# Optimization experiments

Hardware: AMD Instinct MI355X
Metric: run time of the kernel (lower is better)

## Reference

```python
import jax, jax.numpy as jnp
import numpy as np

B, NELEC, D, NION = 2048, 32, 128, 8
NSPIN = 2
NS = NELEC // NSPIN  # electrons (= orbitals) per spin


def setup_inputs() -> dict:
    key = jax.random.key(0)
    ks = jax.random.split(key, 6)
    eq_inputs = jax.random.normal(ks[0], (B, NELEC, D), dtype=jnp.float32)
    r_ei = jax.random.normal(ks[1], (B, NELEC, NION, 3), dtype=jnp.float32)
    W = jax.random.normal(ks[2], (NSPIN, D, NS), dtype=jnp.float32) / np.sqrt(D).astype(np.float32)
    b = jax.random.normal(ks[3], (NSPIN, NS), dtype=jnp.float32) * 0.1
    env_a = jax.random.normal(ks[4], (NSPIN, NION, NS), dtype=jnp.float32) * 0.5 + 1.0
    env_ion = jax.random.normal(ks[5], (NSPIN, NION, NS), dtype=jnp.float32) / np.sqrt(NION).astype(np.float32)
    return {"eq_inputs": eq_inputs, "r_ei": r_ei, "W": W, "b": b,
            "env_a": env_a, "env_ion": env_ion}


def _submatrix_row_indices(n):
    # idx[i, j] = row index kept at slot j after deleting row i
    j = np.arange(n - 1)
    idx = j[None, :] + (j[None, :] >= np.arange(n)[:, None])
    return jnp.asarray(idx)  # (n, n-1) int32


def reference(eq_inputs, r_ei, W, b, env_a, env_ion):
    # split into spins (equal split -> stack for vectorization)
    eq_s = jnp.stack(jnp.split(eq_inputs, NSPIN, axis=-2))   # (s,B,ns,d)
    rei_s = jnp.stack(jnp.split(r_ei, NSPIN, axis=-3))       # (s,B,ns,nion,3)

    # FermiNet orbital layer: linear part * isotropic exponential envelope
    linear = jnp.einsum("sbnd,sdo->sbno", eq_s, W) + b[:, None, None, :]
    dist = jnp.linalg.norm(rei_s, axis=-1)                   # (s,B,ns,nion)
    # exp(-||a (r - R)||) = exp(-|a| * ||r - R||) for isotropic scalar decay a
    exp_part = jnp.exp(-dist[..., None] * jnp.abs(env_a)[:, None, None, :, :])
    env = jnp.einsum("sbnio,sio->sbno", exp_part, env_ion)
    M = linear * env                                         # (s,B,ns,ns) square orbital matrices

    # slog cofactor antiequivariance along first column
    first = M[..., 0]                                        # (s,B,ns)
    osign = jnp.sign(first)
    olog = jnp.log(jnp.abs(first))
    y = M[..., 1:]                                           # delete column 0
    idx = _submatrix_row_indices(NS)
    sub = jnp.take(y, idx, axis=-2)                          # (s,B,ns,ns-1,ns-1): row i deleted
    csign, clog = jnp.linalg.slogdet(sub)                    # (s,B,ns)
    alt = jnp.asarray((-1.0) ** np.arange(NS), dtype=M.dtype)  # alternating signs (-1)^i
    a_sign = osign * csign * alt
    a_log = olog + clog

    # multiply equivariant inputs (slog form) by the per-particle antisymmetry
    out_sign = jnp.sign(eq_s) * a_sign[..., None]            # (s,B,ns,d)
    out_log = jnp.log(jnp.abs(eq_s)) + a_log[..., None]
    # stacked representation of the per-spin SLArrayList: (spin, {sign,log}, B, ns, d)
    return jnp.stack([out_sign, out_log], axis=1)
```

## Files before the change

### kernel.cpp

```cpp
#include <hip/hip_runtime.h>
#include <math.h>

#define NB 2048

__device__ __forceinline__ float signf_(float x) {
    return (x > 0.0f) ? 1.0f : ((x < 0.0f) ? -1.0f : 0.0f);
}

__global__ __launch_bounds__(256, 3)
void slogcof_kernel(const float* __restrict__ eq,
                    const float* __restrict__ rei,
                    const float* __restrict__ Wm,
                    const float* __restrict__ bias,
                    const float* __restrict__ env_a,
                    const float* __restrict__ env_ion,
                    float* __restrict__ out)
{
    __shared__ float  sEq[4][16][132];
    __shared__ double sM[4][16][18];
    __shared__ double sDist[4][16][8];
    __shared__ float  sA[4][2][16];

    const int tid = threadIdx.x;
    const int w   = tid >> 6;
    const int l   = tid & 63;
    const int P   = blockIdx.x * 4 + w;
    const int s   = P >> 11;
    const int bb  = P & (NB - 1);

    const int o16 = l & 15;
    const int q4  = l >> 4;

    const float* eqp = eq + (size_t)bb * 4096 + s * 2048;
    #pragma unroll
    for (int it = 0; it < 8; ++it) {
        const int idx = it * 256 + l * 4;
        const float4 v = *reinterpret_cast<const float4*>(eqp + idx);
        *reinterpret_cast<float4*>(&sEq[w][idx >> 7][idx & 127]) = v;
    }

    #pragma unroll
    for (int rep = 0; rep < 2; ++rep) {
        const int n = (l >> 3) + rep * 8;
        const int i = l & 7;
        const float* rp = rei + (size_t)bb * 768 + s * 384 + n * 24 + i * 3;
        const double x = (double)rp[0], y = (double)rp[1], z = (double)rp[2];
        sDist[w][n][i] = sqrt(x * x + y * y + z * z);
    }

    __syncthreads();

    double accv[4] = {0.0, 0.0, 0.0, 0.0};
    {
        const float* Wp = Wm + s * 2048;
        #pragma unroll 4
        for (int d0 = 0; d0 < 128; d0 += 4) {
            const float4 a0 = *reinterpret_cast<const float4*>(&sEq[w][4 * q4 + 0][d0]);
            const float4 a1 = *reinterpret_cast<const float4*>(&sEq[w][4 * q4 + 1][d0]);
            const float4 a2 = *reinterpret_cast<const float4*>(&sEq[w][4 * q4 + 2][d0]);
            const float4 a3 = *reinterpret_cast<const float4*>(&sEq[w][4 * q4 + 3][d0]);
            const double w0 = (double)Wp[(d0 + 0) * 16 + o16];
            const double w1 = (double)Wp[(d0 + 1) * 16 + o16];
            const double w2 = (double)Wp[(d0 + 2) * 16 + o16];
            const double w3 = (double)Wp[(d0 + 3) * 16 + o16];
            accv[0] += (double)a0.x * w0 + (double)a0.y * w1 + (double)a0.z * w2 + (double)a0.w * w3;
            accv[1] += (double)a1.x * w0 + (double)a1.y * w1 + (double)a1.z * w2 + (double)a1.w * w3;
            accv[2] += (double)a2.x * w0 + (double)a2.y * w1 + (double)a2.z * w2 + (double)a2.w * w3;
            accv[3] += (double)a3.x * w0 + (double)a3.y * w1 + (double)a3.z * w2 + (double)a3.w * w3;
        }
    }

    {
        const double bd = (double)bias[s * 16 + o16];
        double ev[4] = {0.0, 0.0, 0.0, 0.0};
        #pragma unroll
        for (int i = 0; i < 8; ++i) {
            const double ea = fabs((double)env_a[s * 128 + i * 16 + o16]);
            const double ei = (double)env_ion[s * 128 + i * 16 + o16];
            #pragma unroll
            for (int j = 0; j < 4; ++j)
                ev[j] += exp(-sDist[w][4 * q4 + j][i] * ea) * ei;
        }
        #pragma unroll
        for (int j = 0; j < 4; ++j)
            sM[w][4 * q4 + j][o16] = (accv[j] + bd) * ev[j];
    }
    __syncthreads();

    if (w == 0) {
        const int g = q4;
        const int j = o16;
        double row[16];
        #pragma unroll
        for (int c = 0; c < 16; ++c) row[c] = sM[g][j][c];
        const double m0 = row[0];

        double logdet = 0.0;
        int dsign = 1;
        int used = 0;
        int mystep = -1;

        #pragma unroll
        for (int k = 0; k < 16; ++k) {
            unsigned key;
            {
                const float av = (float)fabs(row[k]);
                key = used ? (unsigned)j
                           : ((__float_as_uint(av) & 0xFFFFFFC0u) | 0x20u | (unsigned)j);
            }
            #pragma unroll
            for (int off = 8; off >= 1; off >>= 1) {
                const unsigned k2 = (unsigned)__shfl_xor((int)key, off, 16);
                if (k2 > key) key = k2;
            }
            const int p = (int)(key & 15u);
            const double pivv = __shfl(row[k], p, 16);
            logdet += (double)logf((float)fabs(pivv));
            if (pivv < 0.0) dsign = -dsign;
            else if (pivv == 0.0) dsign = 0;
            if (j == p) { used = 1; mystep = k; }
            const double minv = (pivv != 0.0) ? (1.0 / pivv) : 0.0;
            const double mul = row[k] * minv;
            const int upd = !used;
            #pragma unroll
            for (int c = k + 1; c < 16; ++c) {
                const double pv = __shfl(row[c], p, 16);
                if (upd) row[c] -= mul * pv;
            }
            if (upd) row[k] = mul;
        }

        int invc = 0;
        #pragma unroll
        for (int j2 = 0; j2 < 16; ++j2) {
            const int s2 = __shfl(mystep, j2, 16);
            if (j2 > j && mystep > s2) invc++;
        }
        #pragma unroll
        for (int off = 8; off >= 1; off >>= 1) invc += __shfl_xor(invc, off, 16);
        if (invc & 1) dsign = -dsign;

        double wv = 0.0;
        #pragma unroll
        for (int o = 0; o < 16; ++o) {
            double c0 = (mystep < o) ? (row[o] * wv) : 0.0;
            #pragma unroll
            for (int off = 8; off >= 1; off >>= 1) c0 += __shfl_xor(c0, off, 16);
            if (mystep == o) wv = (((o == 0) ? 1.0 : 0.0) - c0) / row[o];
        }
        double vv = 0.0;
        #pragma unroll
        for (int k = 15; k >= 0; --k) {
            double c0 = (mystep > k) ? (row[k] * vv) : 0.0;
            #pragma unroll
            for (int off = 8; off >= 1; off >>= 1) c0 += __shfl_xor(c0, off, 16);
            if (mystep == k) vv = wv - c0;
        }

        const double zj = vv;
        const float zs = (zj > 0.0) ? 1.0f : ((zj < 0.0) ? -1.0f : 0.0f);
        const float ms = (m0 > 0.0) ? 1.0f : ((m0 < 0.0) ? -1.0f : 0.0f);
        sA[g][0][j] = ms * (float)dsign * zs;
        sA[g][1][j] = logf((float)fabs(m0)) + (float)logdet + logf((float)fabs(zj));
    }
    __syncthreads();

    float* op0 = out + (size_t)s * 8388608 + (size_t)bb * 2048;
    float* op1 = op0 + 4194304;
    #pragma unroll
    for (int it = 0; it < 8; ++it) {
        const int n  = it * 2 + (l >> 5);
        const int d0 = (l & 31) * 4;
        const float4 x = *reinterpret_cast<const float4*>(&sEq[w][n][d0]);
        const float a_s = sA[w][0][n];
        const float a_l = sA[w][1][n];
        float4 osg, olg;
        osg.x = signf_(x.x) * a_s;  olg.x = logf(fabsf(x.x)) + a_l;
        osg.y = signf_(x.y) * a_s;  olg.y = logf(fabsf(x.y)) + a_l;
        osg.z = signf_(x.z) * a_s;  olg.z = logf(fabsf(x.z)) + a_l;
        osg.w = signf_(x.w) * a_s;  olg.w = logf(fabsf(x.w)) + a_l;
        *reinterpret_cast<float4*>(op0 + n * 128 + d0) = osg;
        *reinterpret_cast<float4*>(op1 + n * 128 + d0) = olg;
    }
}

extern "C" void kernel_launch(void* const* d_in, const int* in_sizes, int n_in,
                              void* d_out, int out_size, void* d_ws, size_t ws_size,
                              hipStream_t stream) {
    (void)in_sizes; (void)n_in; (void)out_size; (void)d_ws; (void)ws_size;
    slogcof_kernel<<<dim3(1024), dim3(256), 0, stream>>>(
        (const float*)d_in[0],
        (const float*)d_in[1],
        (const float*)d_in[2],
        (const float*)d_in[3],
        (const float*)d_in[4],
        (const float*)d_in[5],
        (float*)d_out);
}
```

Before: 143.6 us.

## Drop LDS staging of eq inputs, read from global, and spread determinant across waves

Measured after the change: 152.6 us. 6.3% more time.

```diff
diff --git a/kernel.cpp b/kernel.cpp
--- a/kernel.cpp
+++ b/kernel.cpp
@@ -7,7 +7,7 @@
     return (x > 0.0f) ? 1.0f : ((x < 0.0f) ? -1.0f : 0.0f);
 }
 
-__global__ __launch_bounds__(256, 3)
+__global__ __launch_bounds__(256, 4)
 void slogcof_kernel(const float* __restrict__ eq,
                     const float* __restrict__ rei,
                     const float* __restrict__ Wm,
@@ -16,7 +16,6 @@
                     const float* __restrict__ env_ion,
                     float* __restrict__ out)
 {
-    __shared__ float  sEq[4][16][132];
     __shared__ double sM[4][16][18];
     __shared__ double sDist[4][16][8];
     __shared__ float  sA[4][2][16];
@@ -32,12 +31,6 @@
     const int q4  = l >> 4;
 
     const float* eqp = eq + (size_t)bb * 4096 + s * 2048;
-    #pragma unroll
-    for (int it = 0; it < 8; ++it) {
-        const int idx = it * 256 + l * 4;
-        const float4 v = *reinterpret_cast<const float4*>(eqp + idx);
-        *reinterpret_cast<float4*>(&sEq[w][idx >> 7][idx & 127]) = v;
-    }
 
     #pragma unroll
     for (int rep = 0; rep < 2; ++rep) {
@@ -47,18 +40,21 @@
         const double x = (double)rp[0], y = (double)rp[1], z = (double)rp[2];
         sDist[w][n][i] = sqrt(x * x + y * y + z * z);
     }
-
     __syncthreads();
 
     double accv[4] = {0.0, 0.0, 0.0, 0.0};
     {
         const float* Wp = Wm + s * 2048;
+        const float* r0 = eqp + (4 * q4 + 0) * 128;
+        const float* r1 = eqp + (4 * q4 + 1) * 128;
+        const float* r2 = eqp + (4 * q4 + 2) * 128;
+        const float* r3 = eqp + (4 * q4 + 3) * 128;
         #pragma unroll 4
         for (int d0 = 0; d0 < 128; d0 += 4) {
-            const float4 a0 = *reinterpret_cast<const float4*>(&sEq[w][4 * q4 + 0][d0]);
-            const float4 a1 = *reinterpret_cast<const float4*>(&sEq[w][4 * q4 + 1][d0]);
-            const float4 a2 = *reinterpret_cast<const float4*>(&sEq[w][4 * q4 + 2][d0]);
-            const float4 a3 = *reinterpret_cast<const float4*>(&sEq[w][4 * q4 + 3][d0]);
+            const float4 a0 = *reinterpret_cast<const float4*>(r0 + d0);
+            const float4 a1 = *reinterpret_cast<const float4*>(r1 + d0);
+            const float4 a2 = *reinterpret_cast<const float4*>(r2 + d0);
+            const float4 a3 = *reinterpret_cast<const float4*>(r3 + d0);
             const double w0 = (double)Wp[(d0 + 0) * 16 + o16];
             const double w1 = (double)Wp[(d0 + 1) * 16 + o16];
             const double w2 = (double)Wp[(d0 + 2) * 16 + o16];
@@ -87,12 +83,11 @@
     }
     __syncthreads();
 
-    if (w == 0) {
-        const int g = q4;
+    {
         const int j = o16;
         double row[16];
         #pragma unroll
-        for (int c = 0; c < 16; ++c) row[c] = sM[g][j][c];
+        for (int c = 0; c < 16; ++c) row[c] = sM[w][j][c];
         const double m0 = row[0];
 
         double logdet = 0.0;
@@ -157,11 +152,13 @@
             if (mystep == k) vv = wv - c0;
         }
 
-        const double zj = vv;
-        const float zs = (zj > 0.0) ? 1.0f : ((zj < 0.0) ? -1.0f : 0.0f);
-        const float ms = (m0 > 0.0) ? 1.0f : ((m0 < 0.0) ? -1.0f : 0.0f);
-        sA[g][0][j] = ms * (float)dsign * zs;
-        sA[g][1][j] = logf((float)fabs(m0)) + (float)logdet + logf((float)fabs(zj));
+        if (l < 16) {
+            const double zj = vv;
+            const float zs = (zj > 0.0) ? 1.0f : ((zj < 0.0) ? -1.0f : 0.0f);
+            const float ms = (m0 > 0.0) ? 1.0f : ((m0 < 0.0) ? -1.0f : 0.0f);
+            sA[w][0][j] = ms * (float)dsign * zs;
+            sA[w][1][j] = logf((float)fabs(m0)) + (float)logdet + logf((float)fabs(zj));
+        }
     }
     __syncthreads();
 
@@ -171,7 +168,7 @@
     for (int it = 0; it < 8; ++it) {
         const int n  = it * 2 + (l >> 5);
         const int d0 = (l & 31) * 4;
-        const float4 x = *reinterpret_cast<const float4*>(&sEq[w][n][d0]);
+        const float4 x = *reinterpret_cast<const float4*>(eqp + n * 128 + d0);
         const float a_s = sA[w][0][n];
         const float a_l = sA[w][1][n];
         float4 osg, olg;
```
